# Kernel optimization log

Measured on AMD Instinct MI355X. Metric: run time of the kernel, lower is better.

Reference implementation:

```python
import jax, jax.numpy as jnp
import numpy as np

E, B, D, H, T = 16, 512, 1536, 768, 2  # experts, batch, embed_dim, hidden (=D//2), num_targets


def setup_inputs() -> dict:
    key = jax.random.key(0)
    ks = jax.random.split(key, 6)
    s = 0.02  # init scale
    return {
        "x": jax.random.normal(ks[0], (B, D), jnp.float32),
        "head_idx": jax.random.randint(ks[1], (B,), 0, E, dtype=jnp.int32),
        "W1": jax.random.normal(ks[2], (E, D, H), jnp.float32) * s,
        "b1": jnp.zeros((E, H), jnp.float32),
        "W2": jax.random.normal(ks[3], (E, H, H), jnp.float32) * s,
        "b2": jnp.zeros((E, H), jnp.float32),
        "W3": jax.random.normal(ks[4], (E, H, T), jnp.float32) * s,
        "b3": jnp.zeros((E, T), jnp.float32),
    }


def reference(x, head_idx, W1, b1, W2, b2, W3, b3):
    # Faithful to: out = cat([mlps[attr_k](x[i:i+1]) for i, attr_k in enumerate(head_idx)])
    # i.e. each sample goes through the 3-layer MLP of its selected expert.
    # Vectorized as: run every expert on the full batch, then per-sample select.
    h = jax.nn.relu(jnp.einsum('bd,edh->ebh', x, W1) + b1[:, None, :])   # [E,B,H]
    h = jax.nn.relu(jnp.einsum('ebh,ehk->ebk', h, W2) + b2[:, None, :])  # [E,B,H]
    out_all = jnp.einsum('ebh,eht->ebt', h, W3) + b3[:, None, :]         # [E,B,T]
    return out_all[head_idx, jnp.arange(x.shape[0])]                     # [B,T]
```

## Files before the change

kernel.cpp:

```cpp
#include <hip/hip_runtime.h>


namespace {
constexpr int NE = 16, NB = 512, ND = 1536, NH = 768;
constexpr int CT = 64;
constexpr int KT = 32;
constexpr int NCT = NH / CT;

template<int DIN, int KS>
__global__ __launch_bounds__(256)
void grouped_mm(const float* __restrict__ act,
                const int*   __restrict__ head_idx,
                const float* __restrict__ W,
                float*       __restrict__ part)
{
    constexpr int KLEN = DIN / KS;
    const int bid = blockIdx.x;
    const int e   = bid / (NCT * KS);
    const int rem = bid % (NCT * KS);
    const int j   = rem / KS;
    const int ks  = rem % KS;
    const int tid = threadIdx.x;

    __shared__ int lst[NB];
    __shared__ int n_sh;
    if (tid < 64) {
        int cnt = 0;
        for (int base = 0; base < NB; base += 64) {
            const int h = head_idx[base + tid];
            const unsigned long long m = __ballot(h == e);
            const int pos = cnt + __popcll(m & ((1ull << tid) - 1ull));
            if (h == e) lst[pos] = base + tid;
            cnt += __popcll(m);
        }
        if (tid == 0) n_sh = cnt;
    }
    __syncthreads();
    const int n = n_sh;
    if (n == 0) return;

    const int c0 = j * CT;
    const int k0 = ks * KLEN;
    const float* Wp   = W + ((size_t)e * DIN) * NH;
    float*       outp = part + ((size_t)ks * NB) * NH;

    __shared__ float Ws[KT][CT];
    __shared__ float Xs[KT][64];

    const int cg = tid & 15;
    const int sg = tid >> 4;

    for (int s0 = 0; s0 < n; s0 += 64) {
        float acc[4][4];
        #pragma unroll
        for (int i = 0; i < 4; ++i)
            #pragma unroll
            for (int q = 0; q < 4; ++q) acc[i][q] = 0.f;

        for (int kt = 0; kt < KLEN; kt += KT) {
            __syncthreads();
            {
                const int kk = tid >> 4;
                const int cc = (tid & 15) * 4;
                const float* g = Wp + (size_t)(k0 + kt + kk) * NH + c0 + cc;
                const float4 v0 = *(const float4*)g;
                const float4 v1 = *(const float4*)(g + (size_t)16 * NH);
                *(float4*)&Ws[kk][cc]      = v0;
                *(float4*)&Ws[kk + 16][cc] = v1;
            }
            {
                const int s  = tid & 63;
                const int kq = tid >> 6;
                if (s0 + s < n) {
                    const float* g = act + (size_t)lst[s0 + s] * DIN + k0 + kt + kq * 8;
                    const float4 v0 = *(const float4*)g;
                    const float4 v1 = *(const float4*)(g + 4);
                    Xs[kq*8+0][s] = v0.x; Xs[kq*8+1][s] = v0.y;
                    Xs[kq*8+2][s] = v0.z; Xs[kq*8+3][s] = v0.w;
                    Xs[kq*8+4][s] = v1.x; Xs[kq*8+5][s] = v1.y;
                    Xs[kq*8+6][s] = v1.z; Xs[kq*8+7][s] = v1.w;
                } else {
                    #pragma unroll
                    for (int i = 0; i < 8; ++i) Xs[kq*8+i][s] = 0.f;
                }
            }
            __syncthreads();
            #pragma unroll
            for (int k = 0; k < KT; ++k) {
                const float4 wv = *(const float4*)&Ws[k][cg * 4];
                const float4 xv = *(const float4*)&Xs[k][sg * 4];
                acc[0][0] += xv.x*wv.x; acc[0][1] += xv.x*wv.y; acc[0][2] += xv.x*wv.z; acc[0][3] += xv.x*wv.w;
                acc[1][0] += xv.y*wv.x; acc[1][1] += xv.y*wv.y; acc[1][2] += xv.y*wv.z; acc[1][3] += xv.y*wv.w;
                acc[2][0] += xv.z*wv.x; acc[2][1] += xv.z*wv.y; acc[2][2] += xv.z*wv.z; acc[2][3] += xv.z*wv.w;
                acc[3][0] += xv.w*wv.x; acc[3][1] += xv.w*wv.y; acc[3][2] += xv.w*wv.z; acc[3][3] += xv.w*wv.w;
            }
        }
        #pragma unroll
        for (int si = 0; si < 4; ++si) {
            const int s = s0 + sg * 4 + si;
            if (s < n) {
                float* o = outp + (size_t)lst[s] * NH + c0 + cg * 4;
                *(float4*)o = make_float4(acc[si][0], acc[si][1], acc[si][2], acc[si][3]);
            }
        }
    }
}

__global__ __launch_bounds__(256)
void combine_relu(const float* __restrict__ part,
                  const float* __restrict__ bias,
                  const int*   __restrict__ head_idx,
                  float*       __restrict__ outp)
{
    const int i = blockIdx.x * 256 + threadIdx.x;
    if (i >= NB * NH / 4) return;
    const int b  = i / (NH / 4);
    const int c4 = i % (NH / 4);
    constexpr int STR = NB * NH / 4;
    const float4* P = (const float4*)part;
    const float4 v0 = P[i], v1 = P[i + STR], v2 = P[i + 2*STR], v3 = P[i + 3*STR];
    const int e = head_idx[b];
    const float4 bb = ((const float4*)bias)[e * (NH / 4) + c4];
    float4 o;
    o.x = fmaxf(v0.x + v1.x + v2.x + v3.x + bb.x, 0.f);
    o.y = fmaxf(v0.y + v1.y + v2.y + v3.y + bb.y, 0.f);
    o.z = fmaxf(v0.z + v1.z + v2.z + v3.z + bb.z, 0.f);
    o.w = fmaxf(v0.w + v1.w + v2.w + v3.w + bb.w, 0.f);
    ((float4*)outp)[i] = o;
}

__global__ __launch_bounds__(64)
void final_head(const float* __restrict__ h2p,
                const float* __restrict__ b2,
                const float* __restrict__ W3,
                const float* __restrict__ b3,
                const int*   __restrict__ head_idx,
                float*       __restrict__ out)
{
    const int b    = blockIdx.x;
    const int lane = threadIdx.x;
    const int e    = head_idx[b];
    constexpr size_t STR = (size_t)NB * NH;
    float a0 = 0.f, a1 = 0.f;
    for (int h = lane; h < NH; h += 64) {
        const size_t o = (size_t)b * NH + h;
        float s = h2p[o] + h2p[STR + o] + h2p[2*STR + o] + h2p[3*STR + o] + b2[e * NH + h];
        s = fmaxf(s, 0.f);
        const float2 w = *(const float2*)&W3[((size_t)e * NH + h) * 2];
        a0 += s * w.x;
        a1 += s * w.y;
    }
    #pragma unroll
    for (int off = 32; off > 0; off >>= 1) {
        a0 += __shfl_down(a0, off);
        a1 += __shfl_down(a1, off);
    }
    if (lane == 0) {
        out[b * 2 + 0] = a0 + b3[e * 2 + 0];
        out[b * 2 + 1] = a1 + b3[e * 2 + 1];
    }
}
}

extern "C" void kernel_launch(void* const* d_in, const int* in_sizes, int n_in,
                              void* d_out, int out_size, void* d_ws, size_t ws_size,
                              hipStream_t stream) {
    const float* x   = (const float*)d_in[0];
    const int*   hi  = (const int*)  d_in[1];
    const float* W1  = (const float*)d_in[2];
    const float* b1  = (const float*)d_in[3];
    const float* W2  = (const float*)d_in[4];
    const float* b2  = (const float*)d_in[5];
    const float* W3  = (const float*)d_in[6];
    const float* b3  = (const float*)d_in[7];
    float* out = (float*)d_out;

    float* h1p = (float*)d_ws;
    float* h1  = h1p + (size_t)4 * NB * NH;
    float* h2p = h1  + (size_t)NB * NH;

    grouped_mm<ND, 4><<<NE * NCT * 4, 256, 0, stream>>>(x,  hi, W1, h1p);
    combine_relu<<<(NB * NH / 4 + 255) / 256, 256, 0, stream>>>(h1p, b1, hi, h1);
    grouped_mm<NH, 4><<<NE * NCT * 4, 256, 0, stream>>>(h1, hi, W2, h2p);
    final_head<<<NB, 64, 0, stream>>>(h2p, b2, W3, b3, hi, out);
}
```

Before: 196.4 us.

## Double-buffer grouped GEMM with async global-to-LDS loads and deeper split-K

Splits the reduction dimension 8 ways instead of 4, which doubles the number of blocks in both grouped matmuls. Double-buffers the weight and activation tiles and loads weight tiles straight into shared memory with the async global_load_lds builtin, so the next tile's loads overlap the current tile's FMAs. This also removes one barrier per K-step. The combine and final-head kernels now sum 8 partial buffers, and final_head packs 4 samples per 256-thread block. The h2 partials reuse the h1 partial workspace; the cost is twice the partial-sum traffic through memory.

```diff
diff --git a/kernel.cpp b/kernel.cpp
--- a/kernel.cpp
+++ b/kernel.cpp
@@ -6,15 +6,23 @@
 constexpr int CT = 64;
 constexpr int KT = 32;
 constexpr int NCT = NH / CT;
-
-template<int DIN, int KS>
-__global__ __launch_bounds__(256)
+constexpr int KS = 8;
+
+__device__ __forceinline__ void gload_lds16(const float* g, float* l) {
+    __builtin_amdgcn_global_load_lds(
+        (const __attribute__((address_space(1))) void*)g,
+        (__attribute__((address_space(3))) void*)l, 16, 0, 0);
+}
+
+template<int DIN>
+__global__ __launch_bounds__(256, 4)
 void grouped_mm(const float* __restrict__ act,
                 const int*   __restrict__ head_idx,
                 const float* __restrict__ W,
                 float*       __restrict__ part)
 {
     constexpr int KLEN = DIN / KS;
+    constexpr int NST  = KLEN / KT;
     const int bid = blockIdx.x;
     const int e   = bid / (NCT * KS);
     const int rem = bid % (NCT * KS);
@@ -44,11 +52,16 @@
     const float* Wp   = W + ((size_t)e * DIN) * NH;
     float*       outp = part + ((size_t)ks * NB) * NH;
 
-    __shared__ float Ws[KT][CT];
-    __shared__ float Xs[KT][64];
+    __shared__ float Ws[2][KT][CT];
+    __shared__ float Xs[2][KT][64];
 
     const int cg = tid & 15;
     const int sg = tid >> 4;
+
+    const int w_kk = tid >> 4;
+    const int w_cc = (tid & 15) * 4;
+    const int x_s  = tid & 63;
+    const int x_kq = tid >> 6;
 
     for (int s0 = 0; s0 < n; s0 += 64) {
         float acc[4][4];
@@ -57,44 +70,48 @@
             #pragma unroll
             for (int q = 0; q < 4; ++q) acc[i][q] = 0.f;
 
-        for (int kt = 0; kt < KLEN; kt += KT) {
-            __syncthreads();
-            {
-                const int kk = tid >> 4;
-                const int cc = (tid & 15) * 4;
-                const float* g = Wp + (size_t)(k0 + kt + kk) * NH + c0 + cc;
+        auto stageW = [&](int buf, int kt) {
+            const float* g = Wp + (size_t)(k0 + kt + w_kk) * NH + c0 + w_cc;
+            gload_lds16(g,                     &Ws[buf][w_kk][w_cc]);
+            gload_lds16(g + (size_t)16 * NH,   &Ws[buf][w_kk + 16][w_cc]);
+        };
+        auto stageX = [&](int buf, int kt) {
+            if (s0 + x_s < n) {
+                const float* g = act + (size_t)lst[s0 + x_s] * DIN + k0 + kt + x_kq * 8;
                 const float4 v0 = *(const float4*)g;
-                const float4 v1 = *(const float4*)(g + (size_t)16 * NH);
-                *(float4*)&Ws[kk][cc]      = v0;
-                *(float4*)&Ws[kk + 16][cc] = v1;
-            }
-            {
-                const int s  = tid & 63;
-                const int kq = tid >> 6;
-                if (s0 + s < n) {
-                    const float* g = act + (size_t)lst[s0 + s] * DIN + k0 + kt + kq * 8;
-                    const float4 v0 = *(const float4*)g;
-                    const float4 v1 = *(const float4*)(g + 4);
-                    Xs[kq*8+0][s] = v0.x; Xs[kq*8+1][s] = v0.y;
-                    Xs[kq*8+2][s] = v0.z; Xs[kq*8+3][s] = v0.w;
-                    Xs[kq*8+4][s] = v1.x; Xs[kq*8+5][s] = v1.y;
-                    Xs[kq*8+6][s] = v1.z; Xs[kq*8+7][s] = v1.w;
-                } else {
-                    #pragma unroll
-                    for (int i = 0; i < 8; ++i) Xs[kq*8+i][s] = 0.f;
-                }
-            }
-            __syncthreads();
+                const float4 v1 = *(const float4*)(g + 4);
+                Xs[buf][x_kq*8+0][x_s] = v0.x; Xs[buf][x_kq*8+1][x_s] = v0.y;
+                Xs[buf][x_kq*8+2][x_s] = v0.z; Xs[buf][x_kq*8+3][x_s] = v0.w;
+                Xs[buf][x_kq*8+4][x_s] = v1.x; Xs[buf][x_kq*8+5][x_s] = v1.y;
+                Xs[buf][x_kq*8+6][x_s] = v1.z; Xs[buf][x_kq*8+7][x_s] = v1.w;
+            } else {
+                #pragma unroll
+                for (int i = 0; i < 8; ++i) Xs[buf][x_kq*8+i][x_s] = 0.f;
+            }
+        };
+
+        stageW(0, 0);
+        stageX(0, 0);
+        __syncthreads();
+
+        for (int t = 0; t < NST; ++t) {
+            const int cur = t & 1;
+            if (t + 1 < NST) {
+                stageW(cur ^ 1, (t + 1) * KT);
+                stageX(cur ^ 1, (t + 1) * KT);
+            }
             #pragma unroll
             for (int k = 0; k < KT; ++k) {
-                const float4 wv = *(const float4*)&Ws[k][cg * 4];
-                const float4 xv = *(const float4*)&Xs[k][sg * 4];
+                const float4 wv = *(const float4*)&Ws[cur][k][cg * 4];
+                const float4 xv = *(const float4*)&Xs[cur][k][sg * 4];
                 acc[0][0] += xv.x*wv.x; acc[0][1] += xv.x*wv.y; acc[0][2] += xv.x*wv.z; acc[0][3] += xv.x*wv.w;
                 acc[1][0] += xv.y*wv.x; acc[1][1] += xv.y*wv.y; acc[1][2] += xv.y*wv.z; acc[1][3] += xv.y*wv.w;
                 acc[2][0] += xv.z*wv.x; acc[2][1] += xv.z*wv.y; acc[2][2] += xv.z*wv.z; acc[2][3] += xv.z*wv.w;
                 acc[3][0] += xv.w*wv.x; acc[3][1] += xv.w*wv.y; acc[3][2] += xv.w*wv.z; acc[3][3] += xv.w*wv.w;
             }
+            __syncthreads();
         }
+
         #pragma unroll
         for (int si = 0; si < 4; ++si) {
             const int s = s0 + sg * 4 + si;
@@ -118,18 +135,21 @@
     const int c4 = i % (NH / 4);
     constexpr int STR = NB * NH / 4;
     const float4* P = (const float4*)part;
-    const float4 v0 = P[i], v1 = P[i + STR], v2 = P[i + 2*STR], v3 = P[i + 3*STR];
     const int e = head_idx[b];
     const float4 bb = ((const float4*)bias)[e * (NH / 4) + c4];
+    float sx = bb.x, sy = bb.y, sz = bb.z, sw = bb.w;
+    #pragma unroll
+    for (int ks = 0; ks < KS; ++ks) {
+        const float4 v = P[i + ks * STR];
+        sx += v.x; sy += v.y; sz += v.z; sw += v.w;
+    }
     float4 o;
-    o.x = fmaxf(v0.x + v1.x + v2.x + v3.x + bb.x, 0.f);
-    o.y = fmaxf(v0.y + v1.y + v2.y + v3.y + bb.y, 0.f);
-    o.z = fmaxf(v0.z + v1.z + v2.z + v3.z + bb.z, 0.f);
-    o.w = fmaxf(v0.w + v1.w + v2.w + v3.w + bb.w, 0.f);
+    o.x = fmaxf(sx, 0.f); o.y = fmaxf(sy, 0.f);
+    o.z = fmaxf(sz, 0.f); o.w = fmaxf(sw, 0.f);
     ((float4*)outp)[i] = o;
 }
 
-__global__ __launch_bounds__(64)
+__global__ __launch_bounds__(256)
 void final_head(const float* __restrict__ h2p,
                 const float* __restrict__ b2,
                 const float* __restrict__ W3,
@@ -137,14 +157,16 @@
                 const int*   __restrict__ head_idx,
                 float*       __restrict__ out)
 {
-    const int b    = blockIdx.x;
-    const int lane = threadIdx.x;
+    const int b    = blockIdx.x * 4 + (threadIdx.x >> 6);
+    const int lane = threadIdx.x & 63;
     const int e    = head_idx[b];
     constexpr size_t STR = (size_t)NB * NH;
     float a0 = 0.f, a1 = 0.f;
     for (int h = lane; h < NH; h += 64) {
         const size_t o = (size_t)b * NH + h;
-        float s = h2p[o] + h2p[STR + o] + h2p[2*STR + o] + h2p[3*STR + o] + b2[e * NH + h];
+        float s = b2[e * NH + h];
+        #pragma unroll
+        for (int ks = 0; ks < KS; ++ks) s += h2p[ks * STR + o];
         s = fmaxf(s, 0.f);
         const float2 w = *(const float2*)&W3[((size_t)e * NH + h) * 2];
         a0 += s * w.x;
@@ -176,11 +198,11 @@
     float* out = (float*)d_out;
 
     float* h1p = (float*)d_ws;
-    float* h1  = h1p + (size_t)4 * NB * NH;
-    float* h2p = h1  + (size_t)NB * NH;
-
-    grouped_mm<ND, 4><<<NE * NCT * 4, 256, 0, stream>>>(x,  hi, W1, h1p);
+    float* h1  = h1p + (size_t)KS * NB * NH;
+    float* h2p = h1p;
+
+    grouped_mm<ND><<<NE * NCT * KS, 256, 0, stream>>>(x,  hi, W1, h1p);
     combine_relu<<<(NB * NH / 4 + 255) / 256, 256, 0, stream>>>(h1p, b1, hi, h1);
-    grouped_mm<NH, 4><<<NE * NCT * 4, 256, 0, stream>>>(h1, hi, W2, h2p);
-    final_head<<<NB, 64, 0, stream>>>(h2p, b2, W3, b3, hi, out);
-}
+    grouped_mm<NH><<<NE * NCT * KS, 256, 0, stream>>>(h1, hi, W2, h2p);
+    final_head<<<NB / 4, 256, 0, stream>>>(h2p, b2, W3, b3, hi, out);
+}
```

Result: slower. 580.7 us (+195.7%).
